# Optimization experiments

Hardware: AMD Instinct MI355X
Metric: run time of the kernel (lower is better)

## Reference

```python
import jax, jax.numpy as jnp
import numpy as np

NL = 4   # numLayers (modules are shared across layers)
H = 8    # numSignalHeads; contextAttention has embed_dim=1 with 1 head


def _ln(x, g, b, eps=1e-10):
    m = x.mean(-1, keepdims=True)
    v = ((x - m) ** 2).mean(-1, keepdims=True)
    return (x - m) / jnp.sqrt(v + eps) * g + b


def _forward(signalData, contextualData, Ws, bs, bn_g, bn_b,
             cWq, cWk, cWv, cbq, cbk, cbv, cbias_k, cbias_v, cWo, cbo,
             xWq, xWk, xWv, xbq, xbk, xbv, xbias_k, xbias_v, xWo, xbo,
             W1, b1, W2, b2, W3, b3,
             ln_ff_g, ln_ff_b, ln_cas_g, ln_cas_b, ln_fin_g, ln_fin_b):
    B, S, E = signalData.shape
    dh = E // H
    scale = float(1.0 / np.sqrt(dh))
    # synthesizeContext: Linear(C,18) + BatchNorm1d(18, track_running_stats=False -> batch stats)
    ec = contextualData @ Ws.T + bs                       # (B,18)
    mu = ec.mean(0)
    var = ((ec - mu) ** 2).mean(0)                        # biased var (PyTorch BN)
    ec = (ec - mu) / jnp.sqrt(var + 1e-5) * bn_g + bn_b
    ec = ec[:, :, None]                                   # (B,18,1)
    sig = signalData
    for _ in range(NL):
        # --- self-attention on context: embed_dim=1, 1 head (head_dim=1, scale=1), add_bias_kv ---
        q = ec @ cWq.T + cbq                              # (B,18,1)
        k = jnp.concatenate([ec @ cWk.T + cbk, jnp.broadcast_to(cbias_k, (B, 1, 1))], axis=1)
        v = jnp.concatenate([ec @ cWv.T + cbv, jnp.broadcast_to(cbias_v, (B, 1, 1))], axis=1)
        a = jax.nn.softmax(jnp.einsum('bqd,bkd->bqk', q, k), axis=-1)
        sa = jnp.einsum('bqk,bkd->bqd', a, v) @ cWo.T + cbo
        ec = ec + sa
        # --- cross-attention: query/value = LN(signal) (E), key = context (kdim=1), add_bias_kv ---
        ns = _ln(sig, ln_cas_g, ln_cas_b)
        q = (ns @ xWq.T + xbq).reshape(B, S, H, dh)
        k = jnp.concatenate([ec @ xWk.T + xbk, jnp.broadcast_to(xbias_k, (B, 1, E))], axis=1).reshape(B, S + 1, H, dh)
        v = jnp.concatenate([ns @ xWv.T + xbv, jnp.broadcast_to(xbias_v, (B, 1, E))], axis=1).reshape(B, S + 1, H, dh)
        a = jax.nn.softmax(jnp.einsum('bqhd,bkhd->bhqk', q, k) * scale, axis=-1)
        ca = jnp.einsum('bhqk,bkhd->bqhd', a, v).reshape(B, S, E) @ xWo.T + xbo
        sig = sig + ca
        # --- feed-forward: Linear->SiLU->Linear->SiLU->Linear->SiLU (dropout = identity in eval) ---
        nf = _ln(sig, ln_ff_g, ln_ff_b)
        ff = jax.nn.silu(jax.nn.silu(jax.nn.silu(nf @ W1.T + b1) @ W2.T + b2) @ W3.T + b3)
        sig = sig + ff
    return _ln(sig, ln_fin_g, ln_fin_b)


def setup_inputs() -> dict:
    key = jax.random.key(0)
    ks = iter(jax.random.split(key, 48))
    r = lambda *s: jax.random.normal(next(ks), s, dtype=jnp.float32) * 0.05
    B, S, E, C = 4096, 18, 256, 512
    return dict(
        signalData=jax.random.normal(next(ks), (B, S, E), dtype=jnp.float32),
        contextualData=jax.random.normal(next(ks), (B, C), dtype=jnp.float32),
        Ws=r(18, C), bs=r(18), bn_g=jnp.ones(18, jnp.float32), bn_b=jnp.zeros(18, jnp.float32),
        cWq=r(1, 1), cWk=r(1, 1), cWv=r(1, 1), cbq=r(1), cbk=r(1), cbv=r(1),
        cbias_k=r(1), cbias_v=r(1), cWo=r(1, 1), cbo=r(1),
        xWq=r(E, E), xWk=r(E, 1), xWv=r(E, E), xbq=r(E), xbk=r(E), xbv=r(E),
        xbias_k=r(E), xbias_v=r(E), xWo=r(E, E), xbo=r(E),
        W1=r(32, E), b1=r(32), W2=r(16, 32), b2=r(16), W3=r(E, 16), b3=r(E),
        ln_ff_g=jnp.ones(E, jnp.float32), ln_ff_b=jnp.zeros(E, jnp.float32),
        ln_cas_g=jnp.ones(E, jnp.float32), ln_cas_b=jnp.zeros(E, jnp.float32),
        ln_fin_g=jnp.ones(E, jnp.float32), ln_fin_b=jnp.zeros(E, jnp.float32),
    )


def reference(signalData, contextualData, Ws, bs, bn_g, bn_b,
              cWq, cWk, cWv, cbq, cbk, cbv, cbias_k, cbias_v, cWo, cbo,
              xWq, xWk, xWv, xbq, xbk, xbv, xbias_k, xbias_v, xWo, xbo,
              W1, b1, W2, b2, W3, b3,
              ln_ff_g, ln_ff_b, ln_cas_g, ln_cas_b, ln_fin_g, ln_fin_b):
    return _forward(signalData, contextualData, Ws, bs, bn_g, bn_b,
                    cWq, cWk, cWv, cbq, cbk, cbv, cbias_k, cbias_v, cWo, cbo,
                    xWq, xWk, xWv, xbq, xbk, xbv, xbias_k, xbias_v, xWo, xbo,
                    W1, b1, W2, b2, W3, b3,
                    ln_ff_g, ln_ff_b, ln_cas_g, ln_cas_b, ln_fin_g, ln_fin_b)
```

## Files before the change

kernel.cpp:

```cpp
#include <hip/hip_runtime.h>

typedef unsigned short u16;
typedef __attribute__((ext_vector_type(8))) short bf16x8;
typedef __attribute__((ext_vector_type(4))) float f32x4;
typedef __attribute__((ext_vector_type(4))) unsigned int u32x4;
typedef __attribute__((ext_vector_type(2))) unsigned int u32x2;

#define MROWS 18
#define MT 2
#define SWZ(r,c)  ((c) ^ (((r)&7)<<3))
#define SWZF(r,c) ((c) ^ ((((r)>>2)&3)<<3))
#define SWZV(n,j) ((j) ^ (((n)&3)<<3))
#define SWZP(i,j) ((j) ^ (((i)&3)<<3))

__device__ inline u16 f2bf(float f){
  unsigned int u = __float_as_uint(f);
  return (u16)((u + 0x7fffu + ((u>>16)&1u)) >> 16);
}
__device__ inline unsigned int packbf(float a, float b){
  return (unsigned int)f2bf(a) | ((unsigned int)f2bf(b)<<16);
}
__device__ inline float bfloat_lo(unsigned int u){ return __uint_as_float(u<<16); }
__device__ inline float bfloat_hi(unsigned int u){ return __uint_as_float(u & 0xffff0000u); }
__device__ inline float wred(float v){
  #pragma unroll
  for (int m=1;m<64;m<<=1) v += __shfl_xor(v, m, 64);
  return v;
}
__device__ inline float silu_f(float x){ return x / (1.f + __expf(-x)); }
__device__ inline f32x4 mfma16(bf16x8 a, bf16x8 b, f32x4 c){
  return __builtin_amdgcn_mfma_f32_16x16x32_bf16(a, b, c, 0, 0, 0);
}

struct Params {
  const float *sigIn;
  const float *bn_g, *bn_b;
  const float *cWq,*cWk,*cWv,*cbq,*cbk,*cbv,*cbias_k,*cbias_v,*cWo,*cbo;
  const float *xbv, *xbias_v, *xbo;
  const float *b1,*b2,*b3;
  const float *g_cas,*b_cas,*g_ff,*b_ff,*g_fin,*b_fin;
  const u16 *Wv,*Wo,*Wq3,*W1b,*W2b,*W3p;
  const float *bias3, *ecr, *mu, *rstd;
  float *out;
};

__global__ void k_prep(const float* __restrict__ xWq, const float* __restrict__ xWk,
                       const float* __restrict__ xWv, const float* __restrict__ xWo,
                       const float* __restrict__ xbq, const float* __restrict__ xbk,
                       const float* __restrict__ xbias_k,
                       const float* __restrict__ W1, const float* __restrict__ W2,
                       const float* __restrict__ W3,
                       u16* Wv, u16* Wo, u16* Wq3, u16* W1b, u16* W2b, u16* W3p, float* bias3){
  const int gid = blockIdx.x*blockDim.x + threadIdx.x;
  const int gsz = gridDim.x*blockDim.x;
  for (int i=gid;i<65536;i+=gsz) Wv[i]=f2bf(xWv[i]);
  for (int i=gid;i<65536;i+=gsz) Wo[i]=f2bf(xWo[i]);
  for (int i=gid;i<8192;i+=gsz)  W1b[i]=f2bf(W1[i]);
  for (int i=gid;i<512;i+=gsz)   W2b[i]=f2bf(W2[i]);
  for (int i=gid;i<8192;i+=gsz){ int o=i>>5, k=i&31; W3p[i] = (k<16)? f2bf(W3[o*16+k]) : (u16)0; }
  for (int i=gid;i<8192;i+=gsz){
    int r=i>>8, c=i&255;
    u16 outv = 0;
    if (r<24){
      int h=r&7, sel=r>>3;
      const float* vec = sel==0? xWk : (sel==1? xbk : xbias_k);
      float s=0.f;
      for (int d=0;d<32;++d) s += xWq[(size_t)(h*32+d)*256+c]*vec[h*32+d];
      outv = f2bf(s);
    }
    Wq3[i]=outv;
  }
  for (int i=gid;i<24;i+=gsz){
    int h=i&7, sel=i>>3;
    const float* vec = sel==0? xWk : (sel==1? xbk : xbias_k);
    float s=0.f; for (int d=0;d<32;++d) s += xbq[h*32+d]*vec[h*32+d];
    bias3[i]=s;
  }
}

__global__ void k_ec(const float* __restrict__ ctx, const float* __restrict__ Ws,
                     const float* __restrict__ bs, float* __restrict__ ecr){
  const int wave = threadIdx.x>>6, lane = threadIdx.x&63;
  const int b = blockIdx.x*4 + wave;
  const float* c = ctx + (size_t)b*512 + lane*8;
  const float4 a0 = *(const float4*)c, a1 = *(const float4*)(c+4);
  float cv[8] = {a0.x,a0.y,a0.z,a0.w,a1.x,a1.y,a1.z,a1.w};
  #pragma unroll 1
  for (int j=0;j<18;++j){
    const float* w = Ws + j*512 + lane*8;
    const float4 w0 = *(const float4*)w, w1 = *(const float4*)(w+4);
    float s = cv[0]*w0.x + cv[1]*w0.y + cv[2]*w0.z + cv[3]*w0.w
            + cv[4]*w1.x + cv[5]*w1.y + cv[6]*w1.z + cv[7]*w1.w;
    s = wred(s);
    if (lane==0) ecr[(size_t)b*18 + j] = s + bs[j];
  }
}

__global__ void k_bn(const float* __restrict__ ecr, float* __restrict__ mu, float* __restrict__ rstd){
  __shared__ float red[256];
  const int tid = threadIdx.x;
  for (int j=0;j<18;++j){
    float s=0.f, s2=0.f;
    for (int b=tid;b<4096;b+=256){ float v = ecr[(size_t)b*18+j]; s+=v; s2+=v*v; }
    red[tid]=s; __syncthreads();
    for (int o=128;o>0;o>>=1){ if(tid<o) red[tid]+=red[tid+o]; __syncthreads(); }
    float S = red[0]; __syncthreads();
    red[tid]=s2; __syncthreads();
    for (int o=128;o>0;o>>=1){ if(tid<o) red[tid]+=red[tid+o]; __syncthreads(); }
    float S2 = red[0]; __syncthreads();
    if (tid==0){ float m = S*(1.f/4096.f); float v = S2*(1.f/4096.f) - m*m;
                 mu[j]=m; rstd[j]=rsqrtf(v+1e-5f); }
  }
}

__global__ __launch_bounds__(256, 2) void k_main(Params P){
  __shared__ __attribute__((aligned(16))) float s_sig[MROWS][256];
  __shared__ __attribute__((aligned(16))) u16 s_ns [MROWS][256];
  __shared__ __attribute__((aligned(16))) u16 s_vT [256][32];
  __shared__ __attribute__((aligned(16))) u16 s_p  [8][MROWS][32];
  __shared__ __attribute__((aligned(16))) u16 s_h1 [MROWS][32];
  __shared__ float s_qq[MROWS][24];
  __shared__ float s_ec[MROWS];
  __shared__ float s_inv[8][MROWS];

  const int tid  = threadIdx.x;
  const int wave = tid >> 6;
  const int lane = tid & 63;
  const int lr   = lane & 15;
  const int lkg  = lane >> 4;
  const int kof  = lkg * 8;
  const int dr   = lkg * 4;
  const int b0   = blockIdx.x;

  for (int idx = tid*4; idx < MROWS*256; idx += 256*4){
    const int row = idx >> 8, col = idx & 255;
    const float4 a = *(const float4*)(P.sigIn + (size_t)b0*18*256 + idx);
    *(float4*)&s_sig[row][SWZF(row,col)] = a;
  }
  {
    const int n = tid;
    #pragma unroll
    for (int jp=9; jp<16; ++jp) *(unsigned int*)&s_vT[n][SWZV(n,2*jp)] = 0u;
    s_vT[n][SWZV(n,18)] = f2bf(P.xbias_v[n]);
  }
  if (lane < 36){
    const int h = 2*wave + (lane>=18 ? 1:0);
    const int i = lane - (lane>=18 ? 18:0);
    #pragma unroll
    for (int jp=10; jp<16; ++jp) *(unsigned int*)&s_p[h][i][SWZP(i,2*jp)] = 0u;
  }
  if (tid < MROWS){
    const float raw = P.ecr[(size_t)b0*18 + tid];
    s_ec[tid] = (raw - P.mu[tid]) * P.rstd[tid] * P.bn_g[tid] + P.bn_b[tid];
  }
  __syncthreads();

  auto ln_pass = [&](const float* g, const float* bvec){
    for (int r = wave; r < MROWS; r += 4){
      const int col = lane*4;
      const float4 x = *(const float4*)&s_sig[r][SWZF(r,col)];
      const float m = wred(x.x+x.y+x.z+x.w)*(1.f/256.f);
      const float d0=x.x-m, d1=x.y-m, d2=x.z-m, d3=x.w-m;
      const float rs = rsqrtf(wred(d0*d0+d1*d1+d2*d2+d3*d3)*(1.f/256.f)+1e-10f);
      const float4 gv = *(const float4*)(g+col);
      const float4 bv = *(const float4*)(bvec+col);
      u32x2 o;
      o[0] = packbf(d0*rs*gv.x+bv.x, d1*rs*gv.y+bv.y);
      o[1] = packbf(d2*rs*gv.z+bv.z, d3*rs*gv.w+bv.w);
      *(u32x2*)&s_ns[r][SWZ(r,col)] = o;
    }
  };

  for (int layer = 0; layer < 4; ++layer){
    float newec = 0.f;
    if (tid < MROWS){
      const int i = tid;
      const float cwq=P.cWq[0], cbq=P.cbq[0], cwk=P.cWk[0], cbk=P.cbk[0];
      const float cwv=P.cWv[0], cbv=P.cbv[0], ck1=P.cbias_k[0], cv1=P.cbias_v[0];
      const float cwo=P.cWo[0], cbo=P.cbo[0];
      const float qi = s_ec[i]*cwq + cbq;
      float mx = qi*ck1;
      #pragma unroll
      for (int j=0;j<18;++j) mx = fmaxf(mx, qi*(s_ec[j]*cwk + cbk));
      float den=0.f, o=0.f;
      #pragma unroll
      for (int j=0;j<18;++j){
        const float pp=__expf(qi*(s_ec[j]*cwk + cbk)-mx);
        den+=pp; o+=pp*(s_ec[j]*cwv+cbv);
      }
      const float pp=__expf(qi*ck1-mx); den+=pp; o+=pp*cv1;
      newec = s_ec[i] + (o/den)*cwo + cbo;
    }
    __syncthreads();
    if (tid < MROWS) s_ec[tid] = newec;

    ln_pass(P.g_cas, P.b_cas);
    __syncthreads();

    {
      f32x4 accV[MT][4]; f32x4 accQ[MT];
      #pragma unroll
      for (int mt=0;mt<MT;++mt){
        accQ[mt] = f32x4{0.f,0.f,0.f,0.f};
        #pragma unroll
        for (int nt=0;nt<4;++nt) accV[mt][nt] = f32x4{0.f,0.f,0.f,0.f};
      }
      for (int kk=0; kk<8; ++kk){
        const int k0 = kk*32 + kof;
        bf16x8 afr[MT];
        #pragma unroll
        for (int mt=0;mt<MT;++mt){
          const int row = mt*16 + lr;
          u32x4 raw = u32x4{0u,0u,0u,0u};
          if (row < MROWS) raw = *(const u32x4*)&s_ns[row][SWZ(row,k0)];
          afr[mt] = __builtin_bit_cast(bf16x8, raw);
        }
        #pragma unroll
        for (int nt=0;nt<4;++nt){
          const int n = (wave*4+nt)*16 + lr;
          const bf16x8 bfr = __builtin_bit_cast(bf16x8, *(const u32x4*)(P.Wv + (size_t)n*256 + k0));
          #pragma unroll
          for (int mt=0;mt<MT;++mt) accV[mt][nt] = mfma16(afr[mt], bfr, accV[mt][nt]);
        }
        if (wave < 2){
          const bf16x8 bq = __builtin_bit_cast(bf16x8, *(const u32x4*)(P.Wq3 + (size_t)(wave*16+lr)*256 + k0));
          #pragma unroll
          for (int mt=0;mt<MT;++mt) accQ[mt] = mfma16(afr[mt], bq, accQ[mt]);
        }
      }
      #pragma unroll
      for (int nt=0;nt<4;++nt){
        const int n = (wave*4+nt)*16 + lr;
        const float bias = P.xbv[n];
        #pragma unroll
        for (int mt=0;mt<MT;++mt){
          #pragma unroll
          for (int q=0;q<4;++q){
            const int row = mt*16 + dr + q;
            if (row < MROWS) s_vT[n][SWZV(n,row)] = f2bf(accV[mt][nt][q] + bias);
          }
        }
      }
      if (wave < 2){
        const int c = wave*16 + lr;
        if (c < 24){
          const float bias = P.bias3[c];
          #pragma unroll
          for (int mt=0;mt<MT;++mt){
            #pragma unroll
            for (int q=0;q<4;++q){
              const int row = mt*16 + dr + q;
              if (row < MROWS) s_qq[row][c] = accQ[mt][q] + bias;
            }
          }
        }
      }
    }
    __syncthreads();

    if (lane < 36){
      const int h = 2*wave + (lane>=18 ? 1:0);
      const int i = lane - (lane>=18 ? 18:0);
      const float scale = 0.17677669529663687f;
      const float qw = s_qq[i][h]*scale, qb = s_qq[i][8+h]*scale, s18 = s_qq[i][16+h]*scale;
      float mx = s18;
      #pragma unroll
      for (int j=0;j<18;++j) mx = fmaxf(mx, qw*s_ec[j] + qb);
      float den = 0.f;
      #pragma unroll
      for (int jj=0;jj<9;++jj){
        const float p0 = __expf(qw*s_ec[2*jj]   + qb - mx);
        const float p1 = __expf(qw*s_ec[2*jj+1] + qb - mx);
        den += p0 + p1;
        *(unsigned int*)&s_p[h][i][SWZP(i,2*jj)] = packbf(p0, p1);
      }
      const float p18 = __expf(s18 - mx); den += p18;
      *(unsigned int*)&s_p[h][i][SWZP(i,18)] = packbf(p18, 0.f);
      s_inv[h][i] = 1.f/den;
    }
    __syncthreads();

    #pragma unroll
    for (int hb=0; hb<2; ++hb){
      const int h = wave*2 + hb;
      const bf16x8 a0 = __builtin_bit_cast(bf16x8, *(const u32x4*)&s_p[h][lr][SWZP(lr,kof)]);
      u32x4 zr = u32x4{0u,0u,0u,0u};
      if (lr < 2) zr = *(const u32x4*)&s_p[h][16+lr][SWZP(16+lr,kof)];
      const bf16x8 a1 = __builtin_bit_cast(bf16x8, zr);
      f32x4 d[MT][2];
      #pragma unroll
      for (int nt=0;nt<2;++nt){
        const int vn = h*32 + nt*16 + lr;
        const bf16x8 b = __builtin_bit_cast(bf16x8, *(const u32x4*)&s_vT[vn][SWZV(vn,kof)]);
        d[0][nt] = mfma16(a0, b, f32x4{0.f,0.f,0.f,0.f});
        d[1][nt] = mfma16(a1, b, f32x4{0.f,0.f,0.f,0.f});
      }
      #pragma unroll
      for (int nt=0;nt<2;++nt){
        #pragma unroll
        for (int mt=0;mt<MT;++mt){
          #pragma unroll
          for (int q=0;q<4;++q){
            const int row = mt*16 + dr + q;
            if (row < MROWS){
              s_ns[row][SWZ(row, h*32 + nt*16 + lr)] = f2bf(d[mt][nt][q]*s_inv[h][row]);
            }
          }
        }
      }
    }
    __syncthreads();

    {
      f32x4 acc[MT][4];
      #pragma unroll
      for (int mt=0;mt<MT;++mt){
        #pragma unroll
        for (int nt=0;nt<4;++nt) acc[mt][nt] = f32x4{0.f,0.f,0.f,0.f};
      }
      for (int kk=0; kk<8; ++kk){
        const int k0 = kk*32 + kof;
        bf16x8 afr[MT];
        #pragma unroll
        for (int mt=0;mt<MT;++mt){
          const int row = mt*16 + lr;
          u32x4 raw = u32x4{0u,0u,0u,0u};
          if (row < MROWS) raw = *(const u32x4*)&s_ns[row][SWZ(row,k0)];
          afr[mt] = __builtin_bit_cast(bf16x8, raw);
        }
        #pragma unroll
        for (int nt=0;nt<4;++nt){
          const int n = (wave*4+nt)*16 + lr;
          const bf16x8 bfr = __builtin_bit_cast(bf16x8, *(const u32x4*)(P.Wo + (size_t)n*256 + k0));
          #pragma unroll
          for (int mt=0;mt<MT;++mt) acc[mt][nt] = mfma16(afr[mt], bfr, acc[mt][nt]);
        }
      }
      #pragma unroll
      for (int nt=0;nt<4;++nt){
        const int n = (wave*4+nt)*16 + lr;
        const float bias = P.xbo[n];
        #pragma unroll
        for (int mt=0;mt<MT;++mt){
          #pragma unroll
          for (int q=0;q<4;++q){
            const int row = mt*16 + dr + q;
            if (row < MROWS) s_sig[row][SWZF(row,n)] += acc[mt][nt][q] + bias;
          }
        }
      }
    }
    __syncthreads();

    ln_pass(P.g_ff, P.b_ff);
    __syncthreads();

    if (wave < 2){
      f32x4 acc[MT];
      #pragma unroll
      for (int mt=0;mt<MT;++mt) acc[mt] = f32x4{0.f,0.f,0.f,0.f};
      for (int kk=0; kk<8; ++kk){
        const int k0 = kk*32 + kof;
        bf16x8 afr[MT];
        #pragma unroll
        for (int mt=0;mt<MT;++mt){
          const int row = mt*16 + lr;
          u32x4 raw = u32x4{0u,0u,0u,0u};
          if (row < MROWS) raw = *(const u32x4*)&s_ns[row][SWZ(row,k0)];
          afr[mt] = __builtin_bit_cast(bf16x8, raw);
        }
        const bf16x8 bfr = __builtin_bit_cast(bf16x8, *(const u32x4*)(P.W1b + (size_t)(wave*16+lr)*256 + k0));
        #pragma unroll
        for (int mt=0;mt<MT;++mt) acc[mt] = mfma16(afr[mt], bfr, acc[mt]);
      }
      const int c = wave*16 + lr;
      const float bias = P.b1[c];
      #pragma unroll
      for (int mt=0;mt<MT;++mt){
        #pragma unroll
        for (int q=0;q<4;++q){
          const int row = mt*16 + dr + q;
          if (row < MROWS) s_h1[row][c] = f2bf(silu_f(acc[mt][q] + bias));
        }
      }
    }
    __syncthreads();

    if (wave < MT){
      const int row_a = wave*16 + lr;
      u32x4 raw = u32x4{0u,0u,0u,0u};
      if (row_a < MROWS) raw = *(const u32x4*)&s_h1[row_a][kof];
      const bf16x8 a = __builtin_bit_cast(bf16x8, raw);
      const bf16x8 b = __builtin_bit_cast(bf16x8, *(const u32x4*)(P.W2b + (size_t)lr*32 + kof));
      f32x4 acc = mfma16(a, b, f32x4{0.f,0.f,0.f,0.f});
      const float bias = P.b2[lr];
      #pragma unroll
      for (int q=0;q<4;++q){
        const int row = wave*16 + dr + q;
        if (row < MROWS){
          s_h1[row][lr]    = f2bf(silu_f(acc[q] + bias));
          s_h1[row][lr+16] = 0;
        }
      }
    }
    __syncthreads();

    {
      bf16x8 afr[MT];
      #pragma unroll
      for (int mt=0;mt<MT;++mt){
        const int row = mt*16 + lr;
        u32x4 raw = u32x4{0u,0u,0u,0u};
        if (row < MROWS) raw = *(const u32x4*)&s_h1[row][kof];
        afr[mt] = __builtin_bit_cast(bf16x8, raw);
      }
      f32x4 acc[MT][4];
      #pragma unroll
      for (int nt=0;nt<4;++nt){
        const int n = (wave*4+nt)*16 + lr;
        const bf16x8 bfr = __builtin_bit_cast(bf16x8, *(const u32x4*)(P.W3p + (size_t)n*32 + kof));
        #pragma unroll
        for (int mt=0;mt<MT;++mt) acc[mt][nt] = mfma16(afr[mt], bfr, f32x4{0.f,0.f,0.f,0.f});
      }
      #pragma unroll
      for (int nt=0;nt<4;++nt){
        const int n = (wave*4+nt)*16 + lr;
        const float b3v = P.b3[n];
        #pragma unroll
        for (int mt=0;mt<MT;++mt){
          #pragma unroll
          for (int q=0;q<4;++q){
            const int row = mt*16 + dr + q;
            if (row < MROWS) s_sig[row][SWZF(row,n)] += silu_f(acc[mt][nt][q] + b3v);
          }
        }
      }
    }
    __syncthreads();
  }

  {
    for (int r = wave; r < MROWS; r += 4){
      const int col = lane*4;
      const float4 x = *(const float4*)&s_sig[r][SWZF(r,col)];
      const float m = wred(x.x+x.y+x.z+x.w)*(1.f/256.f);
      const float d0=x.x-m, d1=x.y-m, d2=x.z-m, d3=x.w-m;
      const float rs = rsqrtf(wred(d0*d0+d1*d1+d2*d2+d3*d3)*(1.f/256.f)+1e-10f);
      const float4 gv = *(const float4*)(P.g_fin+col);
      const float4 bv = *(const float4*)(P.b_fin+col);
      float4 o;
      o.x = d0*rs*gv.x+bv.x; o.y = d1*rs*gv.y+bv.y;
      o.z = d2*rs*gv.z+bv.z; o.w = d3*rs*gv.w+bv.w;
      *(float4*)(P.out + ((size_t)b0*18 + r)*256 + col) = o;
    }
  }
}

extern "C" void kernel_launch(void* const* d_in, const int* in_sizes, int n_in,
                              void* d_out, int out_size, void* d_ws, size_t ws_size,
                              hipStream_t stream) {
  (void)in_sizes; (void)n_in; (void)out_size; (void)ws_size;
  const float* sigIn   = (const float*)d_in[0];
  const float* ctx     = (const float*)d_in[1];
  const float* Ws      = (const float*)d_in[2];
  const float* bs      = (const float*)d_in[3];
  const float* bn_g    = (const float*)d_in[4];
  const float* bn_b    = (const float*)d_in[5];
  const float* cWq     = (const float*)d_in[6];
  const float* cWk     = (const float*)d_in[7];
  const float* cWv     = (const float*)d_in[8];
  const float* cbq     = (const float*)d_in[9];
  const float* cbk     = (const float*)d_in[10];
  const float* cbv     = (const float*)d_in[11];
  const float* cbias_k = (const float*)d_in[12];
  const float* cbias_v = (const float*)d_in[13];
  const float* cWo     = (const float*)d_in[14];
  const float* cbo     = (const float*)d_in[15];
  const float* xWq     = (const float*)d_in[16];
  const float* xWk     = (const float*)d_in[17];
  const float* xWv     = (const float*)d_in[18];
  const float* xbq     = (const float*)d_in[19];
  const float* xbk     = (const float*)d_in[20];
  const float* xbv     = (const float*)d_in[21];
  const float* xbias_k = (const float*)d_in[22];
  const float* xbias_v = (const float*)d_in[23];
  const float* xWo     = (const float*)d_in[24];
  const float* xbo     = (const float*)d_in[25];
  const float* W1      = (const float*)d_in[26];
  const float* b1      = (const float*)d_in[27];
  const float* W2      = (const float*)d_in[28];
  const float* b2      = (const float*)d_in[29];
  const float* W3      = (const float*)d_in[30];
  const float* b3      = (const float*)d_in[31];
  const float* g_ff    = (const float*)d_in[32];
  const float* b_ff    = (const float*)d_in[33];
  const float* g_cas   = (const float*)d_in[34];
  const float* b_cas   = (const float*)d_in[35];
  const float* g_fin   = (const float*)d_in[36];
  const float* b_fin   = (const float*)d_in[37];

  char* ws = (char*)d_ws;
  u16*  Wv    = (u16*)(ws);
  u16*  Wo    = (u16*)(ws + 131072);
  u16*  Wq3   = (u16*)(ws + 262144);
  u16*  W1b   = (u16*)(ws + 278528);
  u16*  W2b   = (u16*)(ws + 294912);
  u16*  W3p   = (u16*)(ws + 295936);
  float* bias3= (float*)(ws + 312320);
  float* ecr  = (float*)(ws + 312448);
  float* mu   = (float*)(ws + 607360);
  float* rstd = (float*)(ws + 607488);

  k_prep<<<dim3(64), dim3(256), 0, stream>>>(xWq, xWk, xWv, xWo, xbq, xbk, xbias_k,
                                             W1, W2, W3, Wv, Wo, Wq3, W1b, W2b, W3p, bias3);
  k_ec<<<dim3(1024), dim3(256), 0, stream>>>(ctx, Ws, bs, ecr);
  k_bn<<<dim3(1), dim3(256), 0, stream>>>(ecr, mu, rstd);

  Params P;
  P.sigIn = sigIn; P.bn_g = bn_g; P.bn_b = bn_b;
  P.cWq=cWq; P.cWk=cWk; P.cWv=cWv; P.cbq=cbq; P.cbk=cbk; P.cbv=cbv;
  P.cbias_k=cbias_k; P.cbias_v=cbias_v; P.cWo=cWo; P.cbo=cbo;
  P.xbv=xbv; P.xbias_v=xbias_v; P.xbo=xbo;
  P.b1=b1; P.b2=b2; P.b3=b3;
  P.g_cas=g_cas; P.b_cas=b_cas; P.g_ff=g_ff; P.b_ff=b_ff; P.g_fin=g_fin; P.b_fin=b_fin;
  P.Wv=Wv; P.Wo=Wo; P.Wq3=Wq3; P.W1b=W1b; P.W2b=W2b; P.W3p=W3p;
  P.bias3=bias3; P.ecr=ecr; P.mu=mu; P.rstd=rstd;
  P.out = (float*)d_out;

  k_main<<<dim3(4096), dim3(256), 0, stream>>>(P);
}
```

Baseline: 1.013 ms.

## Store residual in bf16 LDS, parallelize BN stats, overlap context attention with LN

The residual signal buffer in shared memory changes from fp32 to bf16, halving its LDS footprint, which could allow more blocks per CU. The residual accumulation loses precision on every update, so numerical error may grow across the layers. The context buffer is transposed so the BatchNorm-statistics kernel runs as 18 blocks, one per feature, instead of one. Inside the main kernel, the context self-attention (wave 0) runs alongside the LayerNorm (other waves), one barrier is removed, the two FFN MLP stages are merged under one wave group, and the V stores are vectorized.

```diff
diff --git a/kernel.cpp b/kernel.cpp
--- a/kernel.cpp
+++ b/kernel.cpp
@@ -9,7 +9,6 @@
 #define MROWS 18
 #define MT 2
 #define SWZ(r,c)  ((c) ^ (((r)&7)<<3))
-#define SWZF(r,c) ((c) ^ ((((r)>>2)&3)<<3))
 #define SWZV(n,j) ((j) ^ (((n)&3)<<3))
 #define SWZP(i,j) ((j) ^ (((i)&3)<<3))
 
@@ -22,6 +21,7 @@
 }
 __device__ inline float bfloat_lo(unsigned int u){ return __uint_as_float(u<<16); }
 __device__ inline float bfloat_hi(unsigned int u){ return __uint_as_float(u & 0xffff0000u); }
+__device__ inline float bf2f(u16 h){ return __uint_as_float(((unsigned int)h)<<16); }
 __device__ inline float wred(float v){
   #pragma unroll
   for (int m=1;m<64;m<<=1) v += __shfl_xor(v, m, 64);
@@ -40,7 +40,7 @@
   const float *b1,*b2,*b3;
   const float *g_cas,*b_cas,*g_ff,*b_ff,*g_fin,*b_fin;
   const u16 *Wv,*Wo,*Wq3,*W1b,*W2b,*W3p;
-  const float *bias3, *ecr, *mu, *rstd;
+  const float *bias3, *ecr_t, *mu, *rstd;
   float *out;
 };
 
@@ -79,7 +79,7 @@
 }
 
 __global__ void k_ec(const float* __restrict__ ctx, const float* __restrict__ Ws,
-                     const float* __restrict__ bs, float* __restrict__ ecr){
+                     const float* __restrict__ bs, float* __restrict__ ecr_t){
   const int wave = threadIdx.x>>6, lane = threadIdx.x&63;
   const int b = blockIdx.x*4 + wave;
   const float* c = ctx + (size_t)b*512 + lane*8;
@@ -92,29 +92,27 @@
     float s = cv[0]*w0.x + cv[1]*w0.y + cv[2]*w0.z + cv[3]*w0.w
             + cv[4]*w1.x + cv[5]*w1.y + cv[6]*w1.z + cv[7]*w1.w;
     s = wred(s);
-    if (lane==0) ecr[(size_t)b*18 + j] = s + bs[j];
-  }
-}
-
-__global__ void k_bn(const float* __restrict__ ecr, float* __restrict__ mu, float* __restrict__ rstd){
+    if (lane==0) ecr_t[(size_t)j*4096 + b] = s + bs[j];
+  }
+}
+
+__global__ void k_bn(const float* __restrict__ ecr_t, float* __restrict__ mu, float* __restrict__ rstd){
   __shared__ float red[256];
-  const int tid = threadIdx.x;
-  for (int j=0;j<18;++j){
-    float s=0.f, s2=0.f;
-    for (int b=tid;b<4096;b+=256){ float v = ecr[(size_t)b*18+j]; s+=v; s2+=v*v; }
-    red[tid]=s; __syncthreads();
-    for (int o=128;o>0;o>>=1){ if(tid<o) red[tid]+=red[tid+o]; __syncthreads(); }
-    float S = red[0]; __syncthreads();
-    red[tid]=s2; __syncthreads();
-    for (int o=128;o>0;o>>=1){ if(tid<o) red[tid]+=red[tid+o]; __syncthreads(); }
-    float S2 = red[0]; __syncthreads();
-    if (tid==0){ float m = S*(1.f/4096.f); float v = S2*(1.f/4096.f) - m*m;
-                 mu[j]=m; rstd[j]=rsqrtf(v+1e-5f); }
-  }
+  const int j = blockIdx.x, tid = threadIdx.x;
+  float s=0.f, s2=0.f;
+  for (int b=tid;b<4096;b+=256){ float v = ecr_t[(size_t)j*4096+b]; s+=v; s2+=v*v; }
+  red[tid]=s; __syncthreads();
+  for (int o=128;o>0;o>>=1){ if(tid<o) red[tid]+=red[tid+o]; __syncthreads(); }
+  float S = red[0]; __syncthreads();
+  red[tid]=s2; __syncthreads();
+  for (int o=128;o>0;o>>=1){ if(tid<o) red[tid]+=red[tid+o]; __syncthreads(); }
+  float S2 = red[0];
+  if (tid==0){ float m = S*(1.f/4096.f); float v = S2*(1.f/4096.f) - m*m;
+               mu[j]=m; rstd[j]=rsqrtf(v+1e-5f); }
 }
 
 __global__ __launch_bounds__(256, 2) void k_main(Params P){
-  __shared__ __attribute__((aligned(16))) float s_sig[MROWS][256];
+  __shared__ __attribute__((aligned(16))) u16 s_sig[MROWS][256];
   __shared__ __attribute__((aligned(16))) u16 s_ns [MROWS][256];
   __shared__ __attribute__((aligned(16))) u16 s_vT [256][32];
   __shared__ __attribute__((aligned(16))) u16 s_p  [8][MROWS][32];
@@ -132,15 +130,21 @@
   const int dr   = lkg * 4;
   const int b0   = blockIdx.x;
 
-  for (int idx = tid*4; idx < MROWS*256; idx += 256*4){
+  for (int idx = tid*8; idx < MROWS*256; idx += 256*8){
     const int row = idx >> 8, col = idx & 255;
-    const float4 a = *(const float4*)(P.sigIn + (size_t)b0*18*256 + idx);
-    *(float4*)&s_sig[row][SWZF(row,col)] = a;
+    const float* src = P.sigIn + (size_t)b0*18*256 + idx;
+    const float4 a = *(const float4*)src;
+    const float4 b = *(const float4*)(src+4);
+    u32x4 w;
+    w[0]=packbf(a.x,a.y); w[1]=packbf(a.z,a.w);
+    w[2]=packbf(b.x,b.y); w[3]=packbf(b.z,b.w);
+    *(u32x4*)&s_sig[row][SWZ(row,col)] = w;
   }
   {
     const int n = tid;
+    s_vT[n][SWZV(n,19)] = 0;
     #pragma unroll
-    for (int jp=9; jp<16; ++jp) *(unsigned int*)&s_vT[n][SWZV(n,2*jp)] = 0u;
+    for (int jp=10; jp<16; ++jp) *(unsigned int*)&s_vT[n][SWZV(n,2*jp)] = 0u;
     s_vT[n][SWZV(n,18)] = f2bf(P.xbias_v[n]);
   }
   if (lane < 36){
@@ -150,17 +154,19 @@
     for (int jp=10; jp<16; ++jp) *(unsigned int*)&s_p[h][i][SWZP(i,2*jp)] = 0u;
   }
   if (tid < MROWS){
-    const float raw = P.ecr[(size_t)b0*18 + tid];
+    const float raw = P.ecr_t[(size_t)tid*4096 + b0];
     s_ec[tid] = (raw - P.mu[tid]) * P.rstd[tid] * P.bn_g[tid] + P.bn_b[tid];
   }
   __syncthreads();
 
-  auto ln_pass = [&](const float* g, const float* bvec){
-    for (int r = wave; r < MROWS; r += 4){
+  auto ln_rows = [&](const float* g, const float* bvec, int wbase, int wstep){
+    for (int r = wbase; r < MROWS; r += wstep){
       const int col = lane*4;
-      const float4 x = *(const float4*)&s_sig[r][SWZF(r,col)];
-      const float m = wred(x.x+x.y+x.z+x.w)*(1.f/256.f);
-      const float d0=x.x-m, d1=x.y-m, d2=x.z-m, d3=x.w-m;
+      const u32x2 raw = *(const u32x2*)&s_sig[r][SWZ(r,col)];
+      const float x0 = bfloat_lo(raw[0]), x1 = bfloat_hi(raw[0]);
+      const float x2 = bfloat_lo(raw[1]), x3 = bfloat_hi(raw[1]);
+      const float m = wred(x0+x1+x2+x3)*(1.f/256.f);
+      const float d0=x0-m, d1=x1-m, d2=x2-m, d3=x3-m;
       const float rs = rsqrtf(wred(d0*d0+d1*d1+d2*d2+d3*d3)*(1.f/256.f)+1e-10f);
       const float4 gv = *(const float4*)(g+col);
       const float4 bv = *(const float4*)(bvec+col);
@@ -172,29 +178,28 @@
   };
 
   for (int layer = 0; layer < 4; ++layer){
-    float newec = 0.f;
-    if (tid < MROWS){
-      const int i = tid;
-      const float cwq=P.cWq[0], cbq=P.cbq[0], cwk=P.cWk[0], cbk=P.cbk[0];
-      const float cwv=P.cWv[0], cbv=P.cbv[0], ck1=P.cbias_k[0], cv1=P.cbias_v[0];
-      const float cwo=P.cWo[0], cbo=P.cbo[0];
-      const float qi = s_ec[i]*cwq + cbq;
-      float mx = qi*ck1;
-      #pragma unroll
-      for (int j=0;j<18;++j) mx = fmaxf(mx, qi*(s_ec[j]*cwk + cbk));
-      float den=0.f, o=0.f;
-      #pragma unroll
-      for (int j=0;j<18;++j){
-        const float pp=__expf(qi*(s_ec[j]*cwk + cbk)-mx);
-        den+=pp; o+=pp*(s_ec[j]*cwv+cbv);
-      }
-      const float pp=__expf(qi*ck1-mx); den+=pp; o+=pp*cv1;
-      newec = s_ec[i] + (o/den)*cwo + cbo;
-    }
-    __syncthreads();
-    if (tid < MROWS) s_ec[tid] = newec;
-
-    ln_pass(P.g_cas, P.b_cas);
+    if (wave == 0){
+      if (lane < MROWS){
+        const int i = lane;
+        const float cwq=P.cWq[0], cbq=P.cbq[0], cwk=P.cWk[0], cbk=P.cbk[0];
+        const float cwv=P.cWv[0], cbv=P.cbv[0], ck1=P.cbias_k[0], cv1=P.cbias_v[0];
+        const float cwo=P.cWo[0], cbo=P.cbo[0];
+        const float qi = s_ec[i]*cwq + cbq;
+        float mx = qi*ck1;
+        #pragma unroll
+        for (int j=0;j<18;++j) mx = fmaxf(mx, qi*(s_ec[j]*cwk + cbk));
+        float den=0.f, o=0.f;
+        #pragma unroll
+        for (int j=0;j<18;++j){
+          const float pp=__expf(qi*(s_ec[j]*cwk + cbk)-mx);
+          den+=pp; o+=pp*(s_ec[j]*cwv+cbv);
+        }
+        const float pp=__expf(qi*ck1-mx); den+=pp; o+=pp*cv1;
+        s_ec[i] = s_ec[i] + (o/den)*cwo + cbo;
+      }
+    } else {
+      ln_rows(P.g_cas, P.b_cas, wave-1, 3);
+    }
     __syncthreads();
 
     {
@@ -234,10 +239,15 @@
         const float bias = P.xbv[n];
         #pragma unroll
         for (int mt=0;mt<MT;++mt){
-          #pragma unroll
-          for (int q=0;q<4;++q){
-            const int row = mt*16 + dr + q;
-            if (row < MROWS) s_vT[n][SWZV(n,row)] = f2bf(accV[mt][nt][q] + bias);
+          const int c0 = mt*16 + dr;
+          if (c0 + 3 < MROWS){
+            u32x2 w;
+            w[0] = packbf(accV[mt][nt][0]+bias, accV[mt][nt][1]+bias);
+            w[1] = packbf(accV[mt][nt][2]+bias, accV[mt][nt][3]+bias);
+            *(u32x2*)&s_vT[n][SWZV(n,c0)] = w;
+          } else if (c0 < MROWS){
+            #pragma unroll
+            for (int q=0;q<2;++q) s_vT[n][SWZV(n,c0+q)] = f2bf(accV[mt][nt][q]+bias);
           }
         }
       }
@@ -278,7 +288,6 @@
       *(unsigned int*)&s_p[h][i][SWZP(i,18)] = packbf(p18, 0.f);
       s_inv[h][i] = 1.f/den;
     }
-    __syncthreads();
 
     #pragma unroll
     for (int hb=0; hb<2; ++hb){
@@ -345,61 +354,59 @@
           #pragma unroll
           for (int q=0;q<4;++q){
             const int row = mt*16 + dr + q;
-            if (row < MROWS) s_sig[row][SWZF(row,n)] += acc[mt][nt][q] + bias;
+            if (row < MROWS){
+              const int si = SWZ(row,n);
+              s_sig[row][si] = f2bf(bf2f(s_sig[row][si]) + acc[mt][nt][q] + bias);
+            }
           }
         }
       }
     }
     __syncthreads();
 
-    ln_pass(P.g_ff, P.b_ff);
+    ln_rows(P.g_ff, P.b_ff, wave, 4);
     __syncthreads();
 
     if (wave < 2){
-      f32x4 acc[MT];
-      #pragma unroll
-      for (int mt=0;mt<MT;++mt) acc[mt] = f32x4{0.f,0.f,0.f,0.f};
+      f32x4 acc[2];
+      acc[0] = f32x4{0.f,0.f,0.f,0.f}; acc[1] = f32x4{0.f,0.f,0.f,0.f};
       for (int kk=0; kk<8; ++kk){
         const int k0 = kk*32 + kof;
-        bf16x8 afr[MT];
-        #pragma unroll
-        for (int mt=0;mt<MT;++mt){
-          const int row = mt*16 + lr;
-          u32x4 raw = u32x4{0u,0u,0u,0u};
-          if (row < MROWS) raw = *(const u32x4*)&s_ns[row][SWZ(row,k0)];
-          afr[mt] = __builtin_bit_cast(bf16x8, raw);
-        }
-        const bf16x8 bfr = __builtin_bit_cast(bf16x8, *(const u32x4*)(P.W1b + (size_t)(wave*16+lr)*256 + k0));
-        #pragma unroll
-        for (int mt=0;mt<MT;++mt) acc[mt] = mfma16(afr[mt], bfr, acc[mt]);
-      }
-      const int c = wave*16 + lr;
-      const float bias = P.b1[c];
-      #pragma unroll
-      for (int mt=0;mt<MT;++mt){
+        const int row = wave*16 + lr;
+        u32x4 raw = u32x4{0u,0u,0u,0u};
+        if (row < MROWS) raw = *(const u32x4*)&s_ns[row][SWZ(row,k0)];
+        const bf16x8 afr = __builtin_bit_cast(bf16x8, raw);
+        #pragma unroll
+        for (int nt=0;nt<2;++nt){
+          const bf16x8 bfr = __builtin_bit_cast(bf16x8, *(const u32x4*)(P.W1b + (size_t)(nt*16+lr)*256 + k0));
+          acc[nt] = mfma16(afr, bfr, acc[nt]);
+        }
+      }
+      #pragma unroll
+      for (int nt=0;nt<2;++nt){
+        const int c = nt*16 + lr;
+        const float bias = P.b1[c];
         #pragma unroll
         for (int q=0;q<4;++q){
-          const int row = mt*16 + dr + q;
-          if (row < MROWS) s_h1[row][c] = f2bf(silu_f(acc[mt][q] + bias));
-        }
-      }
-    }
-    __syncthreads();
-
-    if (wave < MT){
-      const int row_a = wave*16 + lr;
-      u32x4 raw = u32x4{0u,0u,0u,0u};
-      if (row_a < MROWS) raw = *(const u32x4*)&s_h1[row_a][kof];
-      const bf16x8 a = __builtin_bit_cast(bf16x8, raw);
-      const bf16x8 b = __builtin_bit_cast(bf16x8, *(const u32x4*)(P.W2b + (size_t)lr*32 + kof));
-      f32x4 acc = mfma16(a, b, f32x4{0.f,0.f,0.f,0.f});
-      const float bias = P.b2[lr];
-      #pragma unroll
-      for (int q=0;q<4;++q){
-        const int row = wave*16 + dr + q;
-        if (row < MROWS){
-          s_h1[row][lr]    = f2bf(silu_f(acc[q] + bias));
-          s_h1[row][lr+16] = 0;
+          const int row = wave*16 + dr + q;
+          if (row < MROWS) s_h1[row][c] = f2bf(silu_f(acc[nt][q] + bias));
+        }
+      }
+      {
+        const int row_a = wave*16 + lr;
+        u32x4 raw = u32x4{0u,0u,0u,0u};
+        if (row_a < MROWS) raw = *(const u32x4*)&s_h1[row_a][kof];
+        const bf16x8 a = __builtin_bit_cast(bf16x8, raw);
+        const bf16x8 b = __builtin_bit_cast(bf16x8, *(const u32x4*)(P.W2b + (size_t)lr*32 + kof));
+        f32x4 acc2 = mfma16(a, b, f32x4{0.f,0.f,0.f,0.f});
+        const float bias = P.b2[lr];
+        #pragma unroll
+        for (int q=0;q<4;++q){
+          const int row = wave*16 + dr + q;
+          if (row < MROWS){
+            s_h1[row][lr]    = f2bf(silu_f(acc2[q] + bias));
+            s_h1[row][lr+16] = 0;
+          }
         }
       }
     }
@@ -431,7 +438,10 @@
           #pragma unroll
           for (int q=0;q<4;++q){
             const int row = mt*16 + dr + q;
-            if (row < MROWS) s_sig[row][SWZF(row,n)] += silu_f(acc[mt][nt][q] + b3v);
+            if (row < MROWS){
+              const int si = SWZ(row,n);
+              s_sig[row][si] = f2bf(bf2f(s_sig[row][si]) + silu_f(acc[mt][nt][q] + b3v));
+            }
           }
         }
       }
@@ -442,9 +452,11 @@
   {
     for (int r = wave; r < MROWS; r += 4){
       const int col = lane*4;
-      const float4 x = *(const float4*)&s_sig[r][SWZF(r,col)];
-      const float m = wred(x.x+x.y+x.z+x.w)*(1.f/256.f);
-      const float d0=x.x-m, d1=x.y-m, d2=x.z-m, d3=x.w-m;
+      const u32x2 raw = *(const u32x2*)&s_sig[r][SWZ(r,col)];
+      const float x0 = bfloat_lo(raw[0]), x1 = bfloat_hi(raw[0]);
+      const float x2 = bfloat_lo(raw[1]), x3 = bfloat_hi(raw[1]);
+      const float m = wred(x0+x1+x2+x3)*(1.f/256.f);
+      const float d0=x0-m, d1=x1-m, d2=x2-m, d3=x3-m;
       const float rs = rsqrtf(wred(d0*d0+d1*d1+d2*d2+d3*d3)*(1.f/256.f)+1e-10f);
       const float4 gv = *(const float4*)(P.g_fin+col);
       const float4 bv = *(const float4*)(P.b_fin+col);
@@ -507,14 +519,14 @@
   u16*  W2b   = (u16*)(ws + 294912);
   u16*  W3p   = (u16*)(ws + 295936);
   float* bias3= (float*)(ws + 312320);
-  float* ecr  = (float*)(ws + 312448);
+  float* ecr_t= (float*)(ws + 312448);
   float* mu   = (float*)(ws + 607360);
   float* rstd = (float*)(ws + 607488);
 
   k_prep<<<dim3(64), dim3(256), 0, stream>>>(xWq, xWk, xWv, xWo, xbq, xbk, xbias_k,
                                              W1, W2, W3, Wv, Wo, Wq3, W1b, W2b, W3p, bias3);
-  k_ec<<<dim3(1024), dim3(256), 0, stream>>>(ctx, Ws, bs, ecr);
-  k_bn<<<dim3(1), dim3(256), 0, stream>>>(ecr, mu, rstd);
+  k_ec<<<dim3(1024), dim3(256), 0, stream>>>(ctx, Ws, bs, ecr_t);
+  k_bn<<<dim3(18), dim3(256), 0, stream>>>(ecr_t, mu, rstd);
 
   Params P;
   P.sigIn = sigIn; P.bn_g = bn_g; P.bn_b = bn_b;
@@ -524,7 +536,7 @@
   P.b1=b1; P.b2=b2; P.b3=b3;
   P.g_cas=g_cas; P.b_cas=b_cas; P.g_ff=g_ff; P.b_ff=b_ff; P.g_fin=g_fin; P.b_fin=b_fin;
   P.Wv=Wv; P.Wo=Wo; P.Wq3=Wq3; P.W1b=W1b; P.W2b=W2b; P.W3p=W3p;
-  P.bias3=bias3; P.ecr=ecr; P.mu=mu; P.rstd=rstd;
+  P.bias3=bias3; P.ecr_t=ecr_t; P.mu=mu; P.rstd=rstd;
   P.out = (float*)d_out;
 
   k_main<<<dim3(4096), dim3(256), 0, stream>>>(P);
```

After: 1.060 ms. 1.05x slower.
